# Optimization experiments

Hardware: AMD Instinct MI355X
Metric: run time of the kernel (lower is better)

## Reference

```python
import jax, jax.numpy as jnp
import numpy as np

IMAGE_SIZE = 1024
PATCH_SIZE = 16
GRID = IMAGE_SIZE // PATCH_SIZE  # 64


def _downsample_nearest(mask, p):
    # torch F.interpolate(mode='nearest') with integer downscale p picks input index i*p
    b = mask.shape[0]
    return mask[:, 0, ::p, ::p].reshape(b, -1)  # (b, N)


def setup_inputs() -> dict:
    key = jax.random.key(0)
    k1, k2, k3, k4 = jax.random.split(key, 4)
    b, N, c = 8, GRID * GRID, 256
    ep_mask_embed = jax.random.normal(k1, (b, N, c), dtype=jnp.float32)
    query_mask_embed = jax.random.normal(k2, (b, N, c), dtype=jnp.float32)
    ep_mask = jax.random.randint(k3, (b, 1, IMAGE_SIZE, IMAGE_SIZE), 0, 2).astype(jnp.float32)
    query_mask = jax.random.randint(k4, (b, 1, IMAGE_SIZE, IMAGE_SIZE), 0, 2).astype(jnp.float32)
    return {"ep_mask_embed": ep_mask_embed, "ep_mask": ep_mask,
            "query_mask_embed": query_mask_embed, "query_mask": query_mask}


def reference(ep_mask_embed, ep_mask, query_mask_embed, query_mask):
    b, N, c = ep_mask_embed.shape
    ep_m = _downsample_nearest(ep_mask, PATCH_SIZE)      # (b, N)
    q_m = _downsample_nearest(query_mask, PATCH_SIZE)    # (b, N)

    # masked episode centers
    pos_center = jnp.einsum('bnc,bn->bc', ep_mask_embed, ep_m) / (jnp.sum(ep_m, -1, keepdims=True) + 0.1)
    rev = 1.0 - ep_m
    neg_center = jnp.einsum('bnc,bn->bc', ep_mask_embed, rev) / (jnp.sum(rev, -1, keepdims=True) + 0.1)

    # per-token squared distance to the corresponding center, summed over channels
    sq_pos = jnp.sum((query_mask_embed - pos_center[:, None, :]) ** 2, axis=-1)  # (b, N)
    sq_neg = jnp.sum((query_mask_embed - neg_center[:, None, :]) ** 2, axis=-1)  # (b, N)

    n_pos = jnp.sum(q_m, axis=-1)            # (b,)
    n_neg = jnp.sum(1.0 - q_m, axis=-1)      # (b,)

    pos_loss = jnp.where(n_pos > 0,
                         jnp.sum(sq_pos * q_m, -1) / (jnp.maximum(n_pos, 1.0) * c),
                         0.0)
    neg_loss = jnp.where(n_neg > 0,
                         jnp.sum(sq_neg * (1.0 - q_m), -1) / (jnp.maximum(n_neg, 1.0) * c),
                         0.0)
    center_loss = pos_loss + neg_loss
    return jnp.stack([jnp.mean(center_loss), jnp.mean(pos_loss), jnp.mean(neg_loss)])
```

## Files before the change

kernel.cpp:

```cpp
#include <hip/hip_runtime.h>

#define BATCH 8
#define NTOK 4096
#define CH 256
#define IMG 1024
#define PATCH 16
#define CHUNKS 32
#define TPB (NTOK / CHUNKS)
#define PART_STRIDE 520
#define NBLK_STATS (2 * BATCH * CHUNKS)
#define SB (NBLK_STATS * PART_STRIDE)


__device__ __forceinline__ float wave_reduce_sum(float v) {
    for (int off = 32; off > 0; off >>= 1) v += __shfl_down(v, off, 64);
    return v;
}

__global__ __launch_bounds__(256) void stats_kernel(
    const float* __restrict__ ep_e, const float* __restrict__ ep_m,
    const float* __restrict__ q_e,  const float* __restrict__ q_m,
    float* __restrict__ ws)
{
    const int bid = blockIdx.x;
    const int tid = threadIdx.x;

    const bool is_q = (bid >= BATCH * CHUNKS);
    const int lb    = bid & (BATCH * CHUNKS - 1);
    const int b     = lb >> 5;
    const int start = (lb & (CHUNKS - 1)) * TPB;

    const float* __restrict__ embed = is_q ? q_e : ep_e;
    const float* __restrict__ mask  = is_q ? q_m : ep_m;

    const int w = tid >> 6, lane = tid & 63, cbase = lane << 2;

    float4 accW = {0.f, 0.f, 0.f, 0.f};
    float4 accS = {0.f, 0.f, 0.f, 0.f};
    float accA = 0.f, accB = 0.f, accm = 0.f;

    const float* ebase = embed + (size_t)(b * NTOK + start) * CH + cbase;
    const size_t mbase = (size_t)b * IMG * IMG;

    const int t0 = w * 32;
    #pragma unroll
    for (int bat = 0; bat < 4; ++bat) {
        float4 e[8];
        float  mm[8];
        #pragma unroll
        for (int k = 0; k < 8; ++k) {
            const int t = t0 + bat * 8 + k;
            const int n = start + t;
            mm[k] = mask[mbase + (size_t)((n >> 6) * PATCH) * IMG + (size_t)((n & 63) * PATCH)];
            e[k]  = *reinterpret_cast<const float4*>(ebase + (size_t)t * CH);
        }
        #pragma unroll
        for (int k = 0; k < 8; ++k) {
            const float m = mm[k];
            accW.x += m * e[k].x; accW.y += m * e[k].y;
            accW.z += m * e[k].z; accW.w += m * e[k].w;
            accS.x += e[k].x;     accS.y += e[k].y;
            accS.z += e[k].z;     accS.w += e[k].w;
            if (is_q) {
                const float d = e[k].x * e[k].x + e[k].y * e[k].y
                              + e[k].z * e[k].z + e[k].w * e[k].w;
                accA += m * d;
                accB += d;
            }
            accm += m;
        }
    }

    __shared__ __align__(16) float ldsW[4][CH];
    __shared__ __align__(16) float ldsS[4][CH];
    __shared__ float ldsA[4], ldsB[4], ldsM[4];

    *reinterpret_cast<float4*>(&ldsW[w][cbase]) = accW;
    *reinterpret_cast<float4*>(&ldsS[w][cbase]) = accS;
    if (is_q) {
        accA = wave_reduce_sum(accA);
        accB = wave_reduce_sum(accB);
    }
    if (lane == 0) { ldsA[w] = accA; ldsB[w] = accB; ldsM[w] = accm; }
    __syncthreads();

    float* p = ws + (size_t)bid * PART_STRIDE;
    const int c = tid;
    p[c]      = ldsW[0][c] + ldsW[1][c] + ldsW[2][c] + ldsW[3][c];
    p[CH + c] = ldsS[0][c] + ldsS[1][c] + ldsS[2][c] + ldsS[3][c];
    if (tid == 0) {
        p[512] = ldsM[0] + ldsM[1] + ldsM[2] + ldsM[3];
        p[513] = is_q ? (ldsA[0] + ldsA[1] + ldsA[2] + ldsA[3]) : 0.f;
        p[514] = is_q ? (ldsB[0] + ldsB[1] + ldsB[2] + ldsB[3]) : 0.f;
    }
}

__global__ __launch_bounds__(256) void mid_kernel(float* __restrict__ ws)
{
    const int b   = blockIdx.x >> 3;
    const int g   = blockIdx.x & 7;
    const int tid = threadIdx.x;
    const int r   = tid >> 5;
    const int c   = tid & 31;
    const int ch  = g * 32 + c;

    float pn = 0.f, se = 0.f, uu = 0.f, vv = 0.f;
    #pragma unroll
    for (int p = 0; p < 4; ++p) {
        const int k = r + 8 * p;
        const float* pe = ws + (size_t)(b * CHUNKS + k) * PART_STRIDE;
        const float* pq = pe + (size_t)(BATCH * CHUNKS) * PART_STRIDE;
        pn += pe[ch]; se += pe[CH + ch];
        uu += pq[ch]; vv += pq[CH + ch];
    }

    __shared__ float s_sc[4];
    if (tid < 32) {
        const float* pe = ws + (size_t)(b * CHUNKS + tid) * PART_STRIDE;
        float v = pe[512];
        #pragma unroll
        for (int off = 16; off; off >>= 1) v += __shfl_xor(v, off, 32);
        if (tid == 0) s_sc[0] = v;
    } else if (tid < 64) {
        const float* pq = ws + (size_t)(BATCH * CHUNKS + b * CHUNKS + (tid - 32)) * PART_STRIDE;
        float n0 = pq[512], a0 = pq[513], b0 = pq[514];
        #pragma unroll
        for (int off = 16; off; off >>= 1) {
            n0 += __shfl_xor(n0, off, 32);
            a0 += __shfl_xor(a0, off, 32);
            b0 += __shfl_xor(b0, off, 32);
        }
        if (tid == 32) { s_sc[1] = n0; s_sc[2] = a0; s_sc[3] = b0; }
    }

    __shared__ float ldsm[4][8][32];
    ldsm[0][r][c] = pn; ldsm[1][r][c] = se;
    ldsm[2][r][c] = uu; ldsm[3][r][c] = vv;
    __syncthreads();

    if (tid < 32) {
        float PN = 0.f, SE = 0.f, UU = 0.f, VV = 0.f;
        #pragma unroll
        for (int rr = 0; rr < 8; ++rr) {
            PN += ldsm[0][rr][tid]; SE += ldsm[1][rr][tid];
            UU += ldsm[2][rr][tid]; VV += ldsm[3][rr][tid];
        }
        const float cnt  = s_sc[0];
        const float id_p = 1.f / (cnt + 0.1f);
        const float id_n = 1.f / (((float)NTOK - cnt) + 0.1f);
        const float pc = PN * id_p;
        const float nc = (SE - PN) * id_n;
        float tx = UU * pc;
        float ty = (VV - UU) * nc;
        float tz = pc * pc;
        float tw = nc * nc;
        #pragma unroll
        for (int off = 16; off; off >>= 1) {
            tx += __shfl_xor(tx, off, 32);
            ty += __shfl_xor(ty, off, 32);
            tz += __shfl_xor(tz, off, 32);
            tw += __shfl_xor(tw, off, 32);
        }
        if (tid == 0) {
            float* o = ws + SB + (size_t)(b * 8 + g) * 8;
            o[0] = tx; o[1] = ty; o[2] = tz; o[3] = tw;
            o[4] = s_sc[0]; o[5] = s_sc[1]; o[6] = s_sc[2]; o[7] = s_sc[3];
        }
    }
}

__global__ __launch_bounds__(64) void tail_kernel(
    const float* __restrict__ ws, float* __restrict__ out)
{
    const int l = threadIdx.x;
    const float* o  = ws + SB + (size_t)l * 8;
    const float* o0 = ws + SB + (size_t)(l & ~7) * 8;
    float tx = o[0], ty = o[1], tz = o[2], tw = o[3];
    const float cnt = o0[4], np = o0[5], A = o0[6], Bv = o0[7];
    (void)cnt;
    #pragma unroll
    for (int off = 4; off; off >>= 1) {
        tx += __shfl_xor(tx, off, 8);
        ty += __shfl_xor(ty, off, 8);
        tz += __shfl_xor(tz, off, 8);
        tw += __shfl_xor(tw, off, 8);
    }
    float pl = 0.f, nl = 0.f;
    if ((l & 7) == 0) {
        const float nn = (float)NTOK - np;
        const float pos_term = A - 2.f * tx + np * tz;
        const float neg_term = (Bv - A) - 2.f * ty + nn * tw;
        pl = (np > 0.f) ? pos_term / (fmaxf(np, 1.f) * (float)CH) : 0.f;
        nl = (nn > 0.f) ? neg_term / (fmaxf(nn, 1.f) * (float)CH) : 0.f;
    }
    #pragma unroll
    for (int off = 32; off; off >>= 1) {
        pl += __shfl_xor(pl, off, 64);
        nl += __shfl_xor(nl, off, 64);
    }
    if (l == 0) {
        const float inv_b = 1.f / (float)BATCH;
        out[0] = (pl + nl) * inv_b;
        out[1] = pl * inv_b;
        out[2] = nl * inv_b;
    }
}

extern "C" void kernel_launch(void* const* d_in, const int* in_sizes, int n_in,
                              void* d_out, int out_size, void* d_ws, size_t ws_size,
                              hipStream_t stream) {
    const float* ep_e = (const float*)d_in[0];
    const float* ep_m = (const float*)d_in[1];
    const float* q_e  = (const float*)d_in[2];
    const float* q_m  = (const float*)d_in[3];
    float* out = (float*)d_out;
    float* ws  = (float*)d_ws;

    stats_kernel<<<NBLK_STATS, 256, 0, stream>>>(ep_e, ep_m, q_e, q_m, ws);
    mid_kernel<<<BATCH * 8, 256, 0, stream>>>(ws);
    tail_kernel<<<1, 64, 0, stream>>>(ws, out);
}
```

Baseline: 22.17 us.

## Fuse stats, mid and tail kernels into one launch with atomic counters

Merges the three kernels into a single launch. Per-batch and global atomic counters let the last-arriving blocks carry out the mid reduction and the final tail, instead of separate dependent launches. This removes two kernel launches and their inter-launch gaps. In exchange it adds a hipMemsetAsync to reset the counters, a spin-wait on other blocks finishing, and relaxed atomic loads and stores for the partials.

```diff
diff --git a/kernel.cpp b/kernel.cpp
--- a/kernel.cpp
+++ b/kernel.cpp
@@ -10,17 +10,22 @@
 #define PART_STRIDE 520
 #define NBLK_STATS (2 * BATCH * CHUNKS)
 #define SB (NBLK_STATS * PART_STRIDE)
-
-
-__device__ __forceinline__ float wave_reduce_sum(float v) {
-    for (int off = 32; off > 0; off >>= 1) v += __shfl_down(v, off, 64);
-    return v;
-}
-
-__global__ __launch_bounds__(256) void stats_kernel(
+#define CNTF (SB + 512)
+
+#define SCOPE __HIP_MEMORY_SCOPE_AGENT
+
+
+__device__ __forceinline__ float aload(const float* p) {
+    return __hip_atomic_load(p, __ATOMIC_RELAXED, SCOPE);
+}
+__device__ __forceinline__ void astore(float* p, float v) {
+    __hip_atomic_store(p, v, __ATOMIC_RELAXED, SCOPE);
+}
+
+__global__ __launch_bounds__(256) void fused_kernel(
     const float* __restrict__ ep_e, const float* __restrict__ ep_m,
     const float* __restrict__ q_e,  const float* __restrict__ q_m,
-    float* __restrict__ ws)
+    float* __restrict__ ws, float* __restrict__ out)
 {
     const int bid = blockIdx.x;
     const int tid = threadIdx.x;
@@ -78,74 +83,93 @@
     *reinterpret_cast<float4*>(&ldsW[w][cbase]) = accW;
     *reinterpret_cast<float4*>(&ldsS[w][cbase]) = accS;
     if (is_q) {
-        accA = wave_reduce_sum(accA);
-        accB = wave_reduce_sum(accB);
+        for (int off = 32; off > 0; off >>= 1) {
+            accA += __shfl_down(accA, off, 64);
+            accB += __shfl_down(accB, off, 64);
+        }
     }
     if (lane == 0) { ldsA[w] = accA; ldsB[w] = accB; ldsM[w] = accm; }
     __syncthreads();
 
     float* p = ws + (size_t)bid * PART_STRIDE;
     const int c = tid;
-    p[c]      = ldsW[0][c] + ldsW[1][c] + ldsW[2][c] + ldsW[3][c];
-    p[CH + c] = ldsS[0][c] + ldsS[1][c] + ldsS[2][c] + ldsS[3][c];
+    astore(&p[c],      ldsW[0][c] + ldsW[1][c] + ldsW[2][c] + ldsW[3][c]);
+    astore(&p[CH + c], ldsS[0][c] + ldsS[1][c] + ldsS[2][c] + ldsS[3][c]);
     if (tid == 0) {
-        p[512] = ldsM[0] + ldsM[1] + ldsM[2] + ldsM[3];
-        p[513] = is_q ? (ldsA[0] + ldsA[1] + ldsA[2] + ldsA[3]) : 0.f;
-        p[514] = is_q ? (ldsB[0] + ldsB[1] + ldsB[2] + ldsB[3]) : 0.f;
-    }
-}
-
-__global__ __launch_bounds__(256) void mid_kernel(float* __restrict__ ws)
-{
-    const int b   = blockIdx.x >> 3;
-    const int g   = blockIdx.x & 7;
-    const int tid = threadIdx.x;
-    const int r   = tid >> 5;
-    const int c   = tid & 31;
-    const int ch  = g * 32 + c;
+        astore(&p[512], ldsM[0] + ldsM[1] + ldsM[2] + ldsM[3]);
+        astore(&p[513], is_q ? (ldsA[0] + ldsA[1] + ldsA[2] + ldsA[3]) : 0.f);
+        astore(&p[514], is_q ? (ldsB[0] + ldsB[1] + ldsB[2] + ldsB[3]) : 0.f);
+    }
+    asm volatile("s_waitcnt vmcnt(0)" ::: "memory");
+    __syncthreads();
+
+    unsigned int* cnt1 = (unsigned int*)(ws + CNTF);
+    unsigned int* cnt2 = (unsigned int*)(ws + CNTF + 8);
+    __shared__ int s_role;
+    if (tid == 0) {
+        unsigned old = __hip_atomic_fetch_add(&cnt1[b], 1u, __ATOMIC_RELAXED, SCOPE);
+        s_role = (old >= 2 * CHUNKS - 8) ? (int)(old - (2 * CHUNKS - 8)) : -1;
+    }
+    __syncthreads();
+    const int g = s_role;
+    if (g < 0) return;
+
+    if (tid == 0) {
+        while (__hip_atomic_load(&cnt1[b], __ATOMIC_RELAXED, SCOPE) < 2u * CHUNKS)
+            __builtin_amdgcn_s_sleep(2);
+    }
+    __syncthreads();
+
+    float* fls = &ldsW[0][0];
+    const int r  = tid >> 5;
+    const int cc = tid & 31;
+    const int ch = g * 32 + cc;
 
     float pn = 0.f, se = 0.f, uu = 0.f, vv = 0.f;
     #pragma unroll
-    for (int p = 0; p < 4; ++p) {
-        const int k = r + 8 * p;
+    for (int pp = 0; pp < 4; ++pp) {
+        const int k = r + 8 * pp;
         const float* pe = ws + (size_t)(b * CHUNKS + k) * PART_STRIDE;
         const float* pq = pe + (size_t)(BATCH * CHUNKS) * PART_STRIDE;
-        pn += pe[ch]; se += pe[CH + ch];
-        uu += pq[ch]; vv += pq[CH + ch];
-    }
-
-    __shared__ float s_sc[4];
+        pn += aload(&pe[ch]); se += aload(&pe[CH + ch]);
+        uu += aload(&pq[ch]); vv += aload(&pq[CH + ch]);
+    }
+
     if (tid < 32) {
         const float* pe = ws + (size_t)(b * CHUNKS + tid) * PART_STRIDE;
-        float v = pe[512];
+        float v = aload(&pe[512]);
         #pragma unroll
         for (int off = 16; off; off >>= 1) v += __shfl_xor(v, off, 32);
-        if (tid == 0) s_sc[0] = v;
+        if (tid == 0) ldsA[0] = v;
     } else if (tid < 64) {
         const float* pq = ws + (size_t)(BATCH * CHUNKS + b * CHUNKS + (tid - 32)) * PART_STRIDE;
-        float n0 = pq[512], a0 = pq[513], b0 = pq[514];
+        float n0 = aload(&pq[512]), a0 = aload(&pq[513]), b0 = aload(&pq[514]);
         #pragma unroll
         for (int off = 16; off; off >>= 1) {
             n0 += __shfl_xor(n0, off, 32);
             a0 += __shfl_xor(a0, off, 32);
             b0 += __shfl_xor(b0, off, 32);
         }
-        if (tid == 32) { s_sc[1] = n0; s_sc[2] = a0; s_sc[3] = b0; }
-    }
-
-    __shared__ float ldsm[4][8][32];
-    ldsm[0][r][c] = pn; ldsm[1][r][c] = se;
-    ldsm[2][r][c] = uu; ldsm[3][r][c] = vv;
-    __syncthreads();
-
+        if (tid == 32) { ldsA[1] = n0; ldsA[2] = a0; ldsA[3] = b0; }
+    }
+
+    fls[0 * 256 + r * 32 + cc] = pn;
+    fls[1 * 256 + r * 32 + cc] = se;
+    fls[2 * 256 + r * 32 + cc] = uu;
+    fls[3 * 256 + r * 32 + cc] = vv;
+    __syncthreads();
+
+    __shared__ int s_tail;
     if (tid < 32) {
         float PN = 0.f, SE = 0.f, UU = 0.f, VV = 0.f;
         #pragma unroll
         for (int rr = 0; rr < 8; ++rr) {
-            PN += ldsm[0][rr][tid]; SE += ldsm[1][rr][tid];
-            UU += ldsm[2][rr][tid]; VV += ldsm[3][rr][tid];
-        }
-        const float cnt  = s_sc[0];
+            PN += fls[0 * 256 + rr * 32 + tid];
+            SE += fls[1 * 256 + rr * 32 + tid];
+            UU += fls[2 * 256 + rr * 32 + tid];
+            VV += fls[3 * 256 + rr * 32 + tid];
+        }
+        const float cnt  = ldsA[0];
         const float id_p = 1.f / (cnt + 0.1f);
         const float id_n = 1.f / (((float)NTOK - cnt) + 0.1f);
         const float pc = PN * id_p;
@@ -163,46 +187,51 @@
         }
         if (tid == 0) {
             float* o = ws + SB + (size_t)(b * 8 + g) * 8;
-            o[0] = tx; o[1] = ty; o[2] = tz; o[3] = tw;
-            o[4] = s_sc[0]; o[5] = s_sc[1]; o[6] = s_sc[2]; o[7] = s_sc[3];
-        }
-    }
-}
-
-__global__ __launch_bounds__(64) void tail_kernel(
-    const float* __restrict__ ws, float* __restrict__ out)
-{
-    const int l = threadIdx.x;
-    const float* o  = ws + SB + (size_t)l * 8;
-    const float* o0 = ws + SB + (size_t)(l & ~7) * 8;
-    float tx = o[0], ty = o[1], tz = o[2], tw = o[3];
-    const float cnt = o0[4], np = o0[5], A = o0[6], Bv = o0[7];
-    (void)cnt;
-    #pragma unroll
-    for (int off = 4; off; off >>= 1) {
-        tx += __shfl_xor(tx, off, 8);
-        ty += __shfl_xor(ty, off, 8);
-        tz += __shfl_xor(tz, off, 8);
-        tw += __shfl_xor(tw, off, 8);
-    }
-    float pl = 0.f, nl = 0.f;
-    if ((l & 7) == 0) {
-        const float nn = (float)NTOK - np;
-        const float pos_term = A - 2.f * tx + np * tz;
-        const float neg_term = (Bv - A) - 2.f * ty + nn * tw;
-        pl = (np > 0.f) ? pos_term / (fmaxf(np, 1.f) * (float)CH) : 0.f;
-        nl = (nn > 0.f) ? neg_term / (fmaxf(nn, 1.f) * (float)CH) : 0.f;
-    }
-    #pragma unroll
-    for (int off = 32; off; off >>= 1) {
-        pl += __shfl_xor(pl, off, 64);
-        nl += __shfl_xor(nl, off, 64);
-    }
-    if (l == 0) {
-        const float inv_b = 1.f / (float)BATCH;
-        out[0] = (pl + nl) * inv_b;
-        out[1] = pl * inv_b;
-        out[2] = nl * inv_b;
+            astore(&o[0], tx); astore(&o[1], ty);
+            astore(&o[2], tz); astore(&o[3], tw);
+            astore(&o[4], ldsA[0]); astore(&o[5], ldsA[1]);
+            astore(&o[6], ldsA[2]); astore(&o[7], ldsA[3]);
+            asm volatile("s_waitcnt vmcnt(0)" ::: "memory");
+            unsigned old2 = __hip_atomic_fetch_add(cnt2, 1u, __ATOMIC_RELAXED, SCOPE);
+            s_tail = (old2 == 8u * BATCH - 1u);
+        }
+    }
+    __syncthreads();
+    if (!s_tail) return;
+
+    if (tid < 64) {
+        const int l = tid;
+        const float* o  = ws + SB + (size_t)l * 8;
+        const float* o0 = ws + SB + (size_t)(l & ~7) * 8;
+        float tx = aload(&o[0]), ty = aload(&o[1]);
+        float tz = aload(&o[2]), tw = aload(&o[3]);
+        const float np = aload(&o0[5]), A = aload(&o0[6]), Bv = aload(&o0[7]);
+        #pragma unroll
+        for (int off = 4; off; off >>= 1) {
+            tx += __shfl_xor(tx, off, 8);
+            ty += __shfl_xor(ty, off, 8);
+            tz += __shfl_xor(tz, off, 8);
+            tw += __shfl_xor(tw, off, 8);
+        }
+        float pl = 0.f, nl = 0.f;
+        if ((l & 7) == 0) {
+            const float nn = (float)NTOK - np;
+            const float pos_term = A - 2.f * tx + np * tz;
+            const float neg_term = (Bv - A) - 2.f * ty + nn * tw;
+            pl = (np > 0.f) ? pos_term / (fmaxf(np, 1.f) * (float)CH) : 0.f;
+            nl = (nn > 0.f) ? neg_term / (fmaxf(nn, 1.f) * (float)CH) : 0.f;
+        }
+        #pragma unroll
+        for (int off = 32; off; off >>= 1) {
+            pl += __shfl_xor(pl, off, 64);
+            nl += __shfl_xor(nl, off, 64);
+        }
+        if (l == 0) {
+            const float inv_b = 1.f / (float)BATCH;
+            out[0] = (pl + nl) * inv_b;
+            out[1] = pl * inv_b;
+            out[2] = nl * inv_b;
+        }
     }
 }
 
@@ -216,7 +245,7 @@
     float* out = (float*)d_out;
     float* ws  = (float*)d_ws;
 
-    stats_kernel<<<NBLK_STATS, 256, 0, stream>>>(ep_e, ep_m, q_e, q_m, ws);
-    mid_kernel<<<BATCH * 8, 256, 0, stream>>>(ws);
-    tail_kernel<<<1, 64, 0, stream>>>(ws, out);
-}
+    hipMemsetAsync((char*)ws + (size_t)CNTF * sizeof(float), 0,
+                   9 * sizeof(unsigned int), stream);
+    fused_kernel<<<NBLK_STATS, 256, 0, stream>>>(ep_e, ep_m, q_e, q_m, ws, out);
+}
```

Result: slower. 32.13 us (+44.9%).
